# Kernel optimization log

Measured on AMD Instinct MI355X. Metric: run time of the kernel, lower is better.

## Reference

```python
import jax, jax.numpy as jnp
import numpy as np

N = 128          # system size (8*8*2), hard-coded in SpectrumLoss
M_LANCZOS = 10   # Lanczos(m=10)
KAPPA = 0.276


def dd_opt(x, U1, kappa):
    # Wilson-style 2D hopping operator (stand-in for the external DDOpt).
    # x: (B,8,8,2) fields, U1: (B,8,8,2) real gauge links (2 directions).
    u0 = U1[..., 0:1]
    u1 = U1[..., 1:2]
    hop = (u0 * jnp.roll(x, -1, axis=1)
           + u1 * jnp.roll(x, -1, axis=2)
           + jnp.roll(u0 * x, 1, axis=1)
           + jnp.roll(u1 * x, 1, axis=2))
    return x - kappa * hop


def build_lower_tri(net_out):
    # Row-major packing of a lower-triangular NxN matrix (torch.tril_indices order).
    B = net_out.shape[0]
    r, c = jnp.tril_indices(N)
    L = jnp.zeros((B, N, N), net_out.dtype)
    return L.at[:, r, c].set(net_out)


def matvect(L, U1, x):
    # x: (B, N). Preconditioned operator: L (L^T (D x)).
    B = x.shape[0]
    y = dd_opt(x.reshape(B, 8, 8, 2), U1, KAPPA).reshape(B, N)
    y = jnp.einsum('bij,bi->bj', L, y)  # upper_tri_mat: M^H v (real -> M^T v)
    y = jnp.einsum('bij,bj->bi', L, y)  # lower_tri_matvect: L v
    return y


def lanczos(Av, v0):
    # Standard batched Lanczos producing symmetric tridiagonal T (B, M, M).
    B = v0.shape[0]

    def step(carry, _):
        v_prev, v_cur, beta = carry
        w = Av(v_cur)
        alpha = jnp.sum(w * v_cur, axis=1)
        w = w - alpha[:, None] * v_cur - beta[:, None] * v_prev
        beta_new = jnp.linalg.norm(w, axis=1)
        v_next = w / (beta_new[:, None] + 1e-30)
        return (v_cur, v_next, beta_new), (alpha, beta_new)

    init = (jnp.zeros_like(v0), v0, jnp.zeros((B,), v0.dtype))
    _, (alphas, betas) = jax.lax.scan(step, init, None, length=M_LANCZOS)
    alphas = alphas.T  # (B, M)
    betas = betas.T    # (B, M); last beta unused
    T = jnp.zeros((B, M_LANCZOS, M_LANCZOS), v0.dtype)
    i = jnp.arange(M_LANCZOS)
    T = T.at[:, i, i].set(alphas)
    j = jnp.arange(M_LANCZOS - 1)
    T = T.at[:, j, j + 1].set(betas[:, :-1])
    T = T.at[:, j + 1, j].set(betas[:, :-1])
    return T


def setup_inputs() -> dict:
    key = jax.random.key(0)
    k1, k2, k3 = jax.random.split(key, 3)
    B = 2048
    net_out = jax.random.normal(k1, (B, N * (N + 1) // 2), dtype=jnp.float32)
    U1 = jax.random.uniform(k2, (B, 8, 8, 2), dtype=jnp.float32)
    v = jax.random.normal(k3, (B, N), dtype=jnp.float32)
    return {"net_out": net_out, "U1": U1, "v": v}


def reference(net_out, U1, v):
    vn = v / jnp.linalg.norm(v, axis=1, keepdims=True)
    L = build_lower_tri(net_out)
    T = lanczos(lambda x: matvect(L, U1, x), vn)
    eig = jnp.abs(jnp.linalg.eigvalsh(T))  # symmetric tridiagonal -> real eigvals
    max_e = jnp.max(eig, axis=1)
    min_e = jnp.min(eig, axis=1)
    return jnp.mean(max_e ** 2) - jnp.mean(min_e ** 2)
```

## Files before the change

### kernel.cpp

```cpp
#include <hip/hip_runtime.h>
#include <hip/hip_bf16.h>
#include <math.h>

#define NN 128
#define TRI 8256
#define BATCH 2048
#define M_L 10
#define KAPPA 0.276f
#define LDL 136

using half8  = __attribute__((ext_vector_type(8))) _Float16;
using half2v = __attribute__((ext_vector_type(2))) _Float16;
using f32x4  = __attribute__((ext_vector_type(4))) float;

static __device__ inline float dot2h(unsigned m, unsigned y, float c) {
#if __has_builtin(__builtin_amdgcn_fdot2)
    return __builtin_amdgcn_fdot2(__builtin_bit_cast(half2v, m),
                                  __builtin_bit_cast(half2v, y), c, false);
#else
    half2v a = __builtin_bit_cast(half2v, m), b = __builtin_bit_cast(half2v, y);
    return c + (float)a.x * (float)b.x + (float)a.y * (float)b.y;
#endif
}

__global__ __launch_bounds__(256, 4) void lanczos_kernel(
    const float* __restrict__ net_out,
    const float* __restrict__ U1,
    const float* __restrict__ v_in,
    float* __restrict__ ab_out)
{
    __shared__ __align__(16) _Float16 Lsq[128 * LDL];
    __shared__ __align__(16) unsigned ys[64];
    __shared__ __align__(16) float part[256];

    const int b = blockIdx.x;
    const int t = threadIdx.x;
    const int lane = t & 63;
    const int w = t >> 6;

    {
        unsigned long long* z = (unsigned long long*)Lsq;
        #pragma unroll
        for (int k = t; k < 128 * LDL / 4; k += 256) z[k] = 0ULL;
    }
    __syncthreads();

    {
        const float4* src4 = (const float4*)(net_out + (size_t)b * TRI);
        for (int q = t; q < TRI / 4; q += 256) {
            float4 f = src4[q];
            int e = 4 * q;
            int r = (int)((sqrtf(8.0f * (float)e + 1.0f) - 1.0f) * 0.5f);
            while ((r + 1) * (r + 2) / 2 <= e) r++;
            while (r * (r + 1) / 2 > e) r--;
            int c = e - r * (r + 1) / 2;
            Lsq[r * LDL + c] = (_Float16)f.x;
            c++; if (c > r) { r++; c = 0; }
            Lsq[r * LDL + c] = (_Float16)f.y;
            c++; if (c > r) { r++; c = 0; }
            Lsq[r * LDL + c] = (_Float16)f.z;
            c++; if (c > r) { r++; c = 0; }
            Lsq[r * LDL + c] = (_Float16)f.w;
        }
    }
    __syncthreads();

    {
        const int m = lane & 15;
        const int g = lane >> 4;
        f32x4 acc[2][8];
        #pragma unroll
        for (int bi = 0; bi < 2; bi++)
            #pragma unroll
            for (int j = 0; j < 8; j++) acc[bi][j] = (f32x4){0.f, 0.f, 0.f, 0.f};
        const int band0 = w, band1 = w + 4;
        #pragma unroll
        for (int kc = 0; kc < 4; kc++) {
            const int col = kc * 32 + g * 8;
            half8 a0 = *(const half8*)&Lsq[(16 * band0 + m) * LDL + col];
            half8 a1 = *(const half8*)&Lsq[(16 * band1 + m) * LDL + col];
            #pragma unroll
            for (int j = 0; j < 8; j++) {
                half8 bfr = *(const half8*)&Lsq[(16 * j + m) * LDL + col];
                acc[0][j] = __builtin_amdgcn_mfma_f32_16x16x32_f16(a0, bfr, acc[0][j], 0, 0, 0);
                acc[1][j] = __builtin_amdgcn_mfma_f32_16x16x32_f16(a1, bfr, acc[1][j], 0, 0, 0);
            }
        }
        __syncthreads();

        #pragma unroll
        for (int bi = 0; bi < 2; bi++) {
            const int band = (bi == 0) ? band0 : band1;
            #pragma unroll
            for (int j = 0; j < 8; j++) {
                f32x4 a = acc[bi][j];
                half2v p01 = {(_Float16)a[0], (_Float16)a[1]};
                half2v p23 = {(_Float16)a[2], (_Float16)a[3]};
                uint2 pk;
                pk.x = __builtin_bit_cast(unsigned, p01);
                pk.y = __builtin_bit_cast(unsigned, p23);
                *(uint2*)&Lsq[(16 * j + m) * LDL + 16 * band + 4 * g] = pk;
            }
        }
    }
    __syncthreads();

    float x0 = 0.f, x1 = 0.f, p0 = 0.f, p1 = 0.f, beta = 0.f;
    float u0c = 0.f, u1c = 0.f, u0m = 0.f, u1m = 0.f;
    const int l_ip = (lane + 8) & 63;
    const int l_jp = (lane & 56) | ((lane + 1) & 7);
    const int l_im = (lane + 56) & 63;
    const int l_jm = (lane & 56) | ((lane + 7) & 7);

    if (w == 0) {
        float2 vv = *(const float2*)(v_in + (size_t)b * NN + 2 * lane);
        float s = vv.x * vv.x + vv.y * vv.y;
        #pragma unroll
        for (int o = 1; o < 64; o <<= 1) s += __shfl_xor(s, o, 64);
        float inv = 1.0f / sqrtf(s);
        x0 = vv.x * inv; x1 = vv.y * inv;
        float2 uu = *(const float2*)(U1 + (size_t)b * 128 + 2 * lane);
        u0c = uu.x; u1c = uu.y;
        u0m = __shfl(u0c, l_im, 64);
        u1m = __shfl(u1c, l_jm, 64);

        float a0 = __shfl(x0, l_ip, 64), a1 = __shfl(x1, l_ip, 64);
        float b0 = __shfl(x0, l_jp, 64), b1 = __shfl(x1, l_jp, 64);
        float c0 = __shfl(x0, l_im, 64), c1 = __shfl(x1, l_im, 64);
        float d0 = __shfl(x0, l_jm, 64), d1 = __shfl(x1, l_jm, 64);
        float y0 = x0 - KAPPA * (u0c * a0 + u1c * b0 + u0m * c0 + u1m * d0);
        float y1 = x1 - KAPPA * (u0c * a1 + u1c * b1 + u0m * c1 + u1m * d1);
        half2v yp = {(_Float16)y0, (_Float16)y1};
        ys[lane] = __builtin_bit_cast(unsigned, yp);
    }
    __syncthreads();

    const int r = t & 127, h = t >> 7;
    const uint4* M4 = (const uint4*)&Lsq[r * LDL + 64 * h];
    const uint4* Y4 = (const uint4*)&ys[32 * h];

    for (int it = 0; it < M_L; it++) {
        {
            float aA = 0.f, aB = 0.f, aC = 0.f, aD = 0.f;
            #pragma unroll
            for (int c = 0; c < 8; c += 4) {
                uint4 m_0 = M4[c],     y_0 = Y4[c];
                uint4 m_1 = M4[c + 1], y_1 = Y4[c + 1];
                uint4 m_2 = M4[c + 2], y_2 = Y4[c + 2];
                uint4 m_3 = M4[c + 3], y_3 = Y4[c + 3];
                aA = dot2h(m_0.x, y_0.x, aA); aA = dot2h(m_0.y, y_0.y, aA);
                aA = dot2h(m_0.z, y_0.z, aA); aA = dot2h(m_0.w, y_0.w, aA);
                aB = dot2h(m_1.x, y_1.x, aB); aB = dot2h(m_1.y, y_1.y, aB);
                aB = dot2h(m_1.z, y_1.z, aB); aB = dot2h(m_1.w, y_1.w, aB);
                aC = dot2h(m_2.x, y_2.x, aC); aC = dot2h(m_2.y, y_2.y, aC);
                aC = dot2h(m_2.z, y_2.z, aC); aC = dot2h(m_2.w, y_2.w, aC);
                aD = dot2h(m_3.x, y_3.x, aD); aD = dot2h(m_3.y, y_3.y, aD);
                aD = dot2h(m_3.z, y_3.z, aD); aD = dot2h(m_3.w, y_3.w, aD);
            }
            part[t] = (aA + aB) + (aC + aD);
        }
        __syncthreads();

        if (w == 0) {
            float2 pa = *(const float2*)&part[2 * lane];
            float2 pb = *(const float2*)&part[128 + 2 * lane];
            float z0 = pa.x + pb.x;
            float z1 = pa.y + pb.y;

            float s1 = z0 * x0 + z1 * x1;
            float s2 = z0 * z0 + z1 * z1;
            float s3 = z0 * p0 + z1 * p1;
            #pragma unroll
            for (int o = 1; o < 64; o <<= 1) {
                s1 += __shfl_xor(s1, o, 64);
                s2 += __shfl_xor(s2, o, 64);
                s3 += __shfl_xor(s3, o, 64);
            }
            float alpha = s1;
            float b2 = s2 - alpha * alpha - beta * (2.0f * s3 - beta);
            float bn = sqrtf(fmaxf(b2, 0.0f));
            float w0 = z0 - alpha * x0 - beta * p0;
            float w1 = z1 - alpha * x1 - beta * p1;
            float inv = 1.0f / (bn + 1e-30f);
            p0 = x0; p1 = x1;
            x0 = w0 * inv; x1 = w1 * inv;
            beta = bn;
            if (lane == 0) {
                ab_out[(size_t)b * 20 + it]      = alpha;
                ab_out[(size_t)b * 20 + 10 + it] = bn;
            }

            float a0 = __shfl(x0, l_ip, 64), a1 = __shfl(x1, l_ip, 64);
            float b0 = __shfl(x0, l_jp, 64), b1 = __shfl(x1, l_jp, 64);
            float c0 = __shfl(x0, l_im, 64), c1 = __shfl(x1, l_im, 64);
            float d0 = __shfl(x0, l_jm, 64), d1 = __shfl(x1, l_jm, 64);
            float y0 = x0 - KAPPA * (u0c * a0 + u1c * b0 + u0m * c0 + u1m * d0);
            float y1 = x1 - KAPPA * (u0c * a1 + u1c * b1 + u0m * c1 + u1m * d1);
            half2v yp = {(_Float16)y0, (_Float16)y1};
            ys[lane] = __builtin_bit_cast(unsigned, yp);
        }
        __syncthreads();
    }
}

__device__ inline int sturm_count10(const double* a, const double* off2, double x) {
    double pm = 1.0;
    double p  = a[0] - x;
    int c = (p < 0.0);
    #pragma unroll
    for (int i = 1; i < M_L; i++) {
        double pn = (a[i] - x) * p - off2[i - 1] * pm;
        c += ((pn < 0.0) != (p < 0.0));
        if (fabs(pn) > 1e150) { pn *= 1e-150; p *= 1e-150; }
        pm = p; p = pn;
    }
    return c;
}

__device__ inline double msect_smallest(const double* a, const double* off2,
                                        double lo, double hi, int K, int lane) {
    for (int round = 0; round < 4; round++) {
        double wdt = (hi - lo) * (1.0 / 65.0);
        double x = lo + wdt * (double)(lane + 1);
        int cnt = sturm_count10(a, off2, x);
        unsigned long long mask = __ballot(cnt >= K);
        if (mask == 0ULL) {
            lo = lo + wdt * 64.0;
        } else {
            int p = __ffsll(mask) - 1;
            hi = lo + wdt * (double)(p + 1);
            if (p > 0) lo = lo + wdt * (double)p;
        }
    }
    return 0.5 * (lo + hi);
}

__device__ inline double msect_window(const double* a, const double* off2,
                                      double maxabs, int lane) {
    double lo = 0.0, hi = maxabs;
    for (int round = 0; round < 4; round++) {
        double wdt = (hi - lo) * (1.0 / 65.0);
        double s = lo + wdt * (double)(lane + 1);
        int inwin = sturm_count10(a, off2, s) - sturm_count10(a, off2, -s);
        unsigned long long mask = __ballot(inwin >= 1);
        if (mask == 0ULL) {
            lo = lo + wdt * 64.0;
        } else {
            int p = __ffsll(mask) - 1;
            hi = lo + wdt * (double)(p + 1);
            if (p > 0) lo = lo + wdt * (double)p;
        }
    }
    return 0.5 * (lo + hi);
}

__global__ __launch_bounds__(256) void eig_kernel(
    const float* __restrict__ ab, float* __restrict__ contrib)
{
    const int lane = threadIdx.x & 63;
    const int b = blockIdx.x * 4 + (threadIdx.x >> 6);
    if (b >= BATCH) return;
    const float* p = ab + (size_t)b * 20;
    double a[M_L], off2[M_L - 1], offa[M_L - 1];
    #pragma unroll
    for (int i = 0; i < M_L; i++) a[i] = (double)p[i];
    #pragma unroll
    for (int i = 0; i < M_L - 1; i++) {
        double bb = (double)p[10 + i];
        offa[i] = fabs(bb);
        off2[i] = bb * bb;
    }
    double lo = 1e300, hi = -1e300;
    #pragma unroll
    for (int i = 0; i < M_L; i++) {
        double r = 0.0;
        if (i > 0) r += offa[i - 1];
        if (i < M_L - 1) r += offa[i];
        lo = fmin(lo, a[i] - r);
        hi = fmax(hi, a[i] + r);
    }
    double lmax = msect_smallest(a, off2, lo, hi, M_L, lane);
    double lmin = msect_smallest(a, off2, lo, hi, 1,   lane);
    double maxabs = fmax(fabs(lmax), fabs(lmin));
    double minabs = msect_window(a, off2, maxabs, lane);
    if (lane == 0) contrib[b] = (float)(maxabs * maxabs - minabs * minabs);
}

__global__ __launch_bounds__(1024) void reduce_kernel(
    const float* __restrict__ contrib, float* __restrict__ out)
{
    __shared__ float red[16];
    int t = threadIdx.x;
    float s = contrib[t] + contrib[t + 1024];
    #pragma unroll
    for (int o = 32; o > 0; o >>= 1) s += __shfl_down(s, o, 64);
    if ((t & 63) == 0) red[t >> 6] = s;
    __syncthreads();
    if (t < 64) {
        float r = (t < 16) ? red[t] : 0.0f;
        #pragma unroll
        for (int o = 8; o > 0; o >>= 1) r += __shfl_down(r, o, 64);
        if (t == 0) out[0] = r / (float)BATCH;
    }
}

extern "C" void kernel_launch(void* const* d_in, const int* in_sizes, int n_in,
                              void* d_out, int out_size, void* d_ws, size_t ws_size,
                              hipStream_t stream) {
    const float* net_out = (const float*)d_in[0];
    const float* U1      = (const float*)d_in[1];
    const float* v       = (const float*)d_in[2];
    float* ab      = (float*)d_ws;
    float* contrib = ab + (size_t)BATCH * 20;

    lanczos_kernel<<<BATCH, 256, 0, stream>>>(net_out, U1, v, ab);
    eig_kernel<<<BATCH / 4, 256, 0, stream>>>(ab, contrib);
    reduce_kernel<<<1, 1024, 0, stream>>>(contrib, (float*)d_out);
}
```

Before: 137.6 us.

## Run Lanczos vector update redundantly per wave and keep L rows in registers

Every wave now computes the Lanczos scalar reductions and the next Dirac-applied vector itself, writing it to a private per-wave scratch slot. This removes the second block-wide barrier per iteration, and the partial-sum buffer is double-buffered to avoid the write-after-read hazard. Each thread also caches its 64 fp16 matrix entries in registers rather than rereading them from LDS every iteration. The cost is redundant work in all four waves and much higher register pressure (32 extra VGPRs), which may reduce occupancy under the 256x4 launch bounds.

```diff
diff --git a/kernel.cpp b/kernel.cpp
--- a/kernel.cpp
+++ b/kernel.cpp
@@ -30,8 +30,8 @@
     float* __restrict__ ab_out)
 {
     __shared__ __align__(16) _Float16 Lsq[128 * LDL];
-    __shared__ __align__(16) unsigned ys[64];
-    __shared__ __align__(16) float part[256];
+    __shared__ __align__(16) unsigned yscr[4][64];
+    __shared__ __align__(16) float part[2][256];
 
     const int b = blockIdx.x;
     const int t = threadIdx.x;
@@ -105,14 +105,22 @@
     }
     __syncthreads();
 
-    float x0 = 0.f, x1 = 0.f, p0 = 0.f, p1 = 0.f, beta = 0.f;
-    float u0c = 0.f, u1c = 0.f, u0m = 0.f, u1m = 0.f;
+    const int r = t & 127, h = t >> 7;
+    uint4 mc[8];
+    {
+        const uint4* M4 = (const uint4*)&Lsq[r * LDL + 64 * h];
+        #pragma unroll
+        for (int c = 0; c < 8; c++) mc[c] = M4[c];
+    }
+
     const int l_ip = (lane + 8) & 63;
     const int l_jp = (lane & 56) | ((lane + 1) & 7);
     const int l_im = (lane + 56) & 63;
     const int l_jm = (lane & 56) | ((lane + 7) & 7);
 
-    if (w == 0) {
+    float x0, x1, p0 = 0.f, p1 = 0.f, beta = 0.f;
+    float u0c, u1c, u0m, u1m;
+    {
         float2 vv = *(const float2*)(v_in + (size_t)b * NN + 2 * lane);
         float s = vv.x * vv.x + vv.y * vv.y;
         #pragma unroll
@@ -131,39 +139,36 @@
         float y0 = x0 - KAPPA * (u0c * a0 + u1c * b0 + u0m * c0 + u1m * d0);
         float y1 = x1 - KAPPA * (u0c * a1 + u1c * b1 + u0m * c1 + u1m * d1);
         half2v yp = {(_Float16)y0, (_Float16)y1};
-        ys[lane] = __builtin_bit_cast(unsigned, yp);
-    }
-    __syncthreads();
-
-    const int r = t & 127, h = t >> 7;
-    const uint4* M4 = (const uint4*)&Lsq[r * LDL + 64 * h];
-    const uint4* Y4 = (const uint4*)&ys[32 * h];
+        yscr[w][lane] = __builtin_bit_cast(unsigned, yp);
+    }
+
+    const uint4* Y4 = (const uint4*)&yscr[w][32 * h];
 
     for (int it = 0; it < M_L; it++) {
+        const int pp = it & 1;
+
         {
             float aA = 0.f, aB = 0.f, aC = 0.f, aD = 0.f;
             #pragma unroll
             for (int c = 0; c < 8; c += 4) {
-                uint4 m_0 = M4[c],     y_0 = Y4[c];
-                uint4 m_1 = M4[c + 1], y_1 = Y4[c + 1];
-                uint4 m_2 = M4[c + 2], y_2 = Y4[c + 2];
-                uint4 m_3 = M4[c + 3], y_3 = Y4[c + 3];
-                aA = dot2h(m_0.x, y_0.x, aA); aA = dot2h(m_0.y, y_0.y, aA);
-                aA = dot2h(m_0.z, y_0.z, aA); aA = dot2h(m_0.w, y_0.w, aA);
-                aB = dot2h(m_1.x, y_1.x, aB); aB = dot2h(m_1.y, y_1.y, aB);
-                aB = dot2h(m_1.z, y_1.z, aB); aB = dot2h(m_1.w, y_1.w, aB);
-                aC = dot2h(m_2.x, y_2.x, aC); aC = dot2h(m_2.y, y_2.y, aC);
-                aC = dot2h(m_2.z, y_2.z, aC); aC = dot2h(m_2.w, y_2.w, aC);
-                aD = dot2h(m_3.x, y_3.x, aD); aD = dot2h(m_3.y, y_3.y, aD);
-                aD = dot2h(m_3.z, y_3.z, aD); aD = dot2h(m_3.w, y_3.w, aD);
-            }
-            part[t] = (aA + aB) + (aC + aD);
+                uint4 y_0 = Y4[c],     y_1 = Y4[c + 1];
+                uint4 y_2 = Y4[c + 2], y_3 = Y4[c + 3];
+                aA = dot2h(mc[c].x,     y_0.x, aA); aA = dot2h(mc[c].y,     y_0.y, aA);
+                aA = dot2h(mc[c].z,     y_0.z, aA); aA = dot2h(mc[c].w,     y_0.w, aA);
+                aB = dot2h(mc[c + 1].x, y_1.x, aB); aB = dot2h(mc[c + 1].y, y_1.y, aB);
+                aB = dot2h(mc[c + 1].z, y_1.z, aB); aB = dot2h(mc[c + 1].w, y_1.w, aB);
+                aC = dot2h(mc[c + 2].x, y_2.x, aC); aC = dot2h(mc[c + 2].y, y_2.y, aC);
+                aC = dot2h(mc[c + 2].z, y_2.z, aC); aC = dot2h(mc[c + 2].w, y_2.w, aC);
+                aD = dot2h(mc[c + 3].x, y_3.x, aD); aD = dot2h(mc[c + 3].y, y_3.y, aD);
+                aD = dot2h(mc[c + 3].z, y_3.z, aD); aD = dot2h(mc[c + 3].w, y_3.w, aD);
+            }
+            part[pp][t] = (aA + aB) + (aC + aD);
         }
         __syncthreads();
 
-        if (w == 0) {
-            float2 pa = *(const float2*)&part[2 * lane];
-            float2 pb = *(const float2*)&part[128 + 2 * lane];
+        {
+            float2 pa = *(const float2*)&part[pp][2 * lane];
+            float2 pb = *(const float2*)&part[pp][128 + 2 * lane];
             float z0 = pa.x + pb.x;
             float z1 = pa.y + pb.y;
 
@@ -185,7 +190,7 @@
             p0 = x0; p1 = x1;
             x0 = w0 * inv; x1 = w1 * inv;
             beta = bn;
-            if (lane == 0) {
+            if (t == 0) {
                 ab_out[(size_t)b * 20 + it]      = alpha;
                 ab_out[(size_t)b * 20 + 10 + it] = bn;
             }
@@ -197,9 +202,8 @@
             float y0 = x0 - KAPPA * (u0c * a0 + u1c * b0 + u0m * c0 + u1m * d0);
             float y1 = x1 - KAPPA * (u0c * a1 + u1c * b1 + u0m * c1 + u1m * d1);
             half2v yp = {(_Float16)y0, (_Float16)y1};
-            ys[lane] = __builtin_bit_cast(unsigned, yp);
-        }
-        __syncthreads();
+            yscr[w][lane] = __builtin_bit_cast(unsigned, yp);
+        }
     }
 }
 
```

Result: slower. 144.5 us (+5.0%).
